# Performance work log

Hardware: AMD Instinct MI355X
Metric: run time of the kernel (lower is better)

The kernel has to match this reference:

```python
import jax, jax.numpy as jnp
import numpy as np

B = 1024
D_FEAT = 64
WINDOW_SIZE = 8192
IR_SIZE = 1024
MAX_STEPS = 2799.0


def setup_inputs() -> dict:
    key = jax.random.key(0)
    ks = jax.random.split(key, 8)
    d_in = D_FEAT + 1  # vel_inputs concat K
    return {
        "vel_inputs": jax.random.normal(ks[0], (B, D_FEAT), dtype=jnp.float32),
        "K": jax.random.uniform(ks[1], (B, 1), dtype=jnp.float32) * MAX_STEPS,
        "eps": jax.random.normal(ks[2], (B, WINDOW_SIZE), dtype=jnp.float32),
        "W_coeff": jax.random.normal(ks[3], (d_in, WINDOW_SIZE), dtype=jnp.float32) * 0.02,
        "b_coeff": jnp.zeros((WINDOW_SIZE,), jnp.float32),
        "W_amps": jax.random.normal(ks[4], (d_in, 1), dtype=jnp.float32) * 0.02,
        "b_amps": jnp.zeros((1,), jnp.float32),
        "W_mean": jax.random.normal(ks[5], (d_in, 1), dtype=jnp.float32) * 0.02,
        "b_mean": jnp.zeros((1,), jnp.float32),
    }


def reference(vel_inputs, K, eps, W_coeff, b_coeff, W_amps, b_amps, W_mean, b_mean):
    # --- small MLP heads ---
    x = jnp.concatenate([vel_inputs, K / MAX_STEPS], axis=-1)  # [B, D+1]
    noise_bands = x @ W_coeff + b_coeff                        # [B, W] (magnitudes)
    amps = jax.nn.sigmoid(x @ W_amps + b_amps)                 # [B, 1]
    mean = jnp.tanh(x @ W_mean + b_mean)                       # [B, 1]

    # --- frequency_impulse_response: irfft + hann windowing (padding>0 branch) ---
    ir = jnp.fft.irfft(noise_bands, axis=-1)   # [B, 2*(W-1)] real
    ir = jnp.fft.fftshift(ir, axes=-1)
    ir_len = 2 * (WINDOW_SIZE - 1)             # 16382
    half = (IR_SIZE + 1) // 2                  # 512
    pad = ir_len - IR_SIZE                     # > 0 path
    n = jnp.arange(IR_SIZE, dtype=jnp.float32)
    hann = 0.5 - 0.5 * jnp.cos(2.0 * jnp.pi * n / IR_SIZE)  # tf periodic hann
    window = jnp.concatenate([hann[half:], jnp.zeros((pad,), jnp.float32), hann[:half]])
    ir = window * ir
    fhs = ir_len - (half - 1) + 1              # first_half_start
    she = half + 1                             # second_half_end
    impulse = jnp.concatenate([ir[:, fhs:], ir[:, :she]], axis=-1)  # [B, IR_SIZE-1]
    ir_final = impulse.shape[-1]               # 1023

    # --- noise generation (eps ~ N(0,1) injected for determinism) ---
    noise = mean + eps                         # [B, W]
    noise = noise / jnp.max(noise)             # global max, as in tf code

    # --- fft_convolve: original broadcasts to [B,B,...] then takes [0];
    # equivalent: noise row 0 convolved with every batch's impulse. ---
    conv_len = ir_final + WINDOW_SIZE - 1
    fft_size = int(2 ** np.ceil(np.log2(conv_len)))  # 16384
    a_fft = jnp.fft.rfft(noise[0], n=fft_size)          # [F]
    ir_fft = jnp.fft.rfft(impulse, n=fft_size, axis=-1)  # [B, F]
    conv = jnp.fft.irfft(a_fft[None, :] * ir_fft, axis=-1)  # [B, fft_size]

    # crop_and_compensate_delay ('same')
    start = (ir_final - 1) // 2 - 1            # 510
    cropped = conv[:, start:start + WINDOW_SIZE]  # [B, W]

    # overlap_and_add over a single frame with step W//2 is the identity
    out_noise = amps * cropped                 # [B, W]
    return out_noise, mean
```

## Files before the change

### kernel.cpp

```cpp
#include <hip/hip_runtime.h>
#include <math.h>

#define NB 1024
#define DF 64
#define WIN 8192
#define LIR 16382
#define TBASE 7681
#define NJ 1024
#define INV_MAXSTEPS (1.0f/2799.0f)
#define TWO_PI 6.28318530717958647692f

#define REVLEN 9248
#define SREV 8212

#define BW_ELEMS 1160
#define BW_CHUNKS 145

using short8 = __attribute__((ext_vector_type(8))) short;
using f32x4  = __attribute__((ext_vector_type(4))) float;

static __device__ __forceinline__ short f2bf(float x) {
    unsigned u = __float_as_uint(x);
    unsigned r = (u + 0x7fffu + ((u >> 16) & 1u)) >> 16;
    return (short)r;
}

__global__ void k_head(const float* __restrict__ vel, const float* __restrict__ Kv,
                       const float* __restrict__ Wa, const float* __restrict__ ba,
                       const float* __restrict__ Wm, const float* __restrict__ bm,
                       float* __restrict__ amps, float* __restrict__ mean,
                       float* __restrict__ out_mean) {
    int b = blockIdx.x * 256 + threadIdx.x;
    if (b >= NB) return;
    float sa = ba[0], sm = bm[0];
    #pragma unroll 8
    for (int d = 0; d < DF; ++d) {
        float v = vel[b * DF + d];
        sa = fmaf(v, Wa[d], sa);
        sm = fmaf(v, Wm[d], sm);
    }
    float xk = Kv[b] * INV_MAXSTEPS;
    sa = fmaf(xk, Wa[DF], sa);
    sm = fmaf(xk, Wm[DF], sm);
    amps[b] = 1.0f / (1.0f + expf(-sa));
    float m = tanhf(sm);
    mean[b] = m;
    out_mean[b] = m;
}

#define PREP_CT_BLK 4096
#define PREP_W_BLK  320
__global__ __launch_bounds__(256) void k_prep(const float* __restrict__ Wc,
                                              const float* __restrict__ bc,
                                              short* __restrict__ Ct,
                                              short* __restrict__ Waug) {
    int bx = blockIdx.x, tid = threadIdx.x;
    if (bx < PREP_CT_BLK) {
        int flat = bx * 2048 + tid * 8;
        int j = flat >> 13, k0 = flat & 8191;
        int t = TBASE + j;
        int p = (k0 * t) % LIR;
        float hw = 0.5f - 0.5f * __builtin_amdgcn_cosf((float)(j + 2) * (1.0f / 1024.0f));
        if (j == NJ - 1) hw = 0.0f;
        short8 v;
        #pragma unroll
        for (int e = 0; e < 8; ++e) {
            int k = k0 + e;
            float w = (k == 0 || k == LIR / 2) ? (1.0f / (float)LIR) : (2.0f / (float)LIR);
            float c = __builtin_amdgcn_cosf((float)p * (1.0f / (float)LIR)) * w * hw;
            v[e] = f2bf(c);
            p += t; if (p >= LIR) p -= LIR;
        }
        *(short8*)(Ct + flat) = v;
    } else {
        int flat = (bx - PREP_CT_BLK) * 2048 + tid * 8;
        int d = flat >> 13, k0 = flat & 8191;
        short8 v;
        #pragma unroll
        for (int e = 0; e < 8; ++e) {
            float x = 0.0f;
            if (d < 65)       x = Wc[(size_t)d * WIN + k0 + e];
            else if (d == 65) x = bc[k0 + e];
            v[e] = f2bf(x);
        }
        *(short8*)(Waug + flat) = v;
    }
}

__global__ void k_maxpart(const float* __restrict__ eps, const float* __restrict__ mean,
                          float* __restrict__ pmax) {
    __shared__ float red[256];
    int tid = threadIdx.x;
    float m = -INFINITY;
    const int total4 = NB * WIN / 4;
    const int stride = 1024 * 256;
    const float4* e4 = (const float4*)eps;
    for (int idx = blockIdx.x * 256 + tid; idx < total4; idx += stride) {
        int b = idx >> 11;
        float4 v = e4[idx];
        float mm = fmaxf(fmaxf(v.x, v.y), fmaxf(v.z, v.w));
        m = fmaxf(m, mean[b] + mm);
    }
    red[tid] = m;
    __syncthreads();
    for (int s = 128; s > 0; s >>= 1) {
        if (tid < s) red[tid] = fmaxf(red[tid], red[tid + s]);
        __syncthreads();
    }
    if (tid == 0) pmax[blockIdx.x] = red[0];
}

__global__ void k_gmax(const float* __restrict__ pmax, const float* __restrict__ mean,
                       float* __restrict__ gmb) {
    __shared__ float red[256];
    int tid = threadIdx.x;
    float m = fmaxf(fmaxf(pmax[tid], pmax[tid + 256]),
                    fmaxf(pmax[tid + 512], pmax[tid + 768]));
    red[tid] = m;
    __syncthreads();
    for (int s = 128; s > 0; s >>= 1) {
        if (tid < s) red[tid] = fmaxf(red[tid], red[tid + s]);
        __syncthreads();
    }
    if (tid == 0) { gmb[0] = 1.0f / red[0]; gmb[1] = mean[0]; }
}

__global__ void k_nrevm(const float* __restrict__ gmb, const float* __restrict__ eps,
                        short* __restrict__ revc) {
    int c = blockIdx.y;
    int x = blockIdx.x * 256 + threadIdx.x;
    if (x >= REVLEN) return;
    float inv = gmb[0], m0 = gmb[1];
    int q = 9239 - x - c;
    int mm = q - 517;
    float v = ((unsigned)mm < (unsigned)WIN) ? (m0 + eps[mm]) * inv : 0.0f;
    revc[c * REVLEN + x] = f2bf(v);
}

#define GA_KCH 256
__global__ __launch_bounds__(256) void k_gemmA(const short* __restrict__ Ct,
                                               const short* __restrict__ Waug,
                                               float* __restrict__ Apart) {
    int tid = threadIdx.x;
    int l = tid & 63, w = tid >> 6;
    int lm = l & 15, lg = l >> 4;
    int m0 = blockIdx.x * 128 + w * 32;
    int ky = blockIdx.y;
    int k0 = ky * GA_KCH;

    const short* pa[2];
    #pragma unroll
    for (int mf = 0; mf < 2; ++mf)
        pa[mf] = Ct + (size_t)(m0 + mf * 16 + lm) * WIN + k0 + 8 * lg;
    const short* pb[5];
    #pragma unroll
    for (int nf = 0; nf < 5; ++nf)
        pb[nf] = Waug + (size_t)(nf * 16 + lm) * WIN + k0 + 8 * lg;

    f32x4 acc[2][5];
    #pragma unroll
    for (int mf = 0; mf < 2; ++mf)
        #pragma unroll
        for (int nf = 0; nf < 5; ++nf)
            #pragma unroll
            for (int r = 0; r < 4; ++r) acc[mf][nf][r] = 0.0f;

    #pragma unroll 2
    for (int kk = 0; kk < GA_KCH; kk += 32) {
        short8 a0 = *(const short8*)(pa[0] + kk);
        short8 a1 = *(const short8*)(pa[1] + kk);
        short8 bb[5];
        #pragma unroll
        for (int nf = 0; nf < 5; ++nf) bb[nf] = *(const short8*)(pb[nf] + kk);
        #pragma unroll
        for (int nf = 0; nf < 5; ++nf) {
            acc[0][nf] = __builtin_amdgcn_mfma_f32_16x16x32_bf16(a0, bb[nf], acc[0][nf], 0, 0, 0);
            acc[1][nf] = __builtin_amdgcn_mfma_f32_16x16x32_bf16(a1, bb[nf], acc[1][nf], 0, 0, 0);
        }
    }
    float* base = Apart + (size_t)ky * (NJ * 80);
    #pragma unroll
    for (int mf = 0; mf < 2; ++mf)
        #pragma unroll
        for (int r = 0; r < 4; ++r) {
            int j = m0 + mf * 16 + 4 * lg + r;
            #pragma unroll
            for (int nf = 0; nf < 5; ++nf)
                base[(size_t)j * 80 + nf * 16 + lm] = acc[mf][nf][r];
        }
}

__global__ __launch_bounds__(256) void k_red(const float* __restrict__ Apart,
                                             float* __restrict__ Aimp) {
    int flat = blockIdx.x * 256 + threadIdx.x;
    float s = 0.0f;
    #pragma unroll 8
    for (int ky = 0; ky < 32; ++ky)
        s += Apart[(size_t)ky * (NJ * 80) + flat];
    int j = flat / 80, d = flat - j * 80;
    Aimp[d * NJ + j] = s;
}

__global__ void k_imp(const float* __restrict__ Aimp, const float* __restrict__ vel,
                      const float* __restrict__ Kv, short* __restrict__ imp_bf) {
    int tid = threadIdx.x;
    int b0 = blockIdx.x * 4;
    float acc[4][4];
    #pragma unroll
    for (int bb = 0; bb < 4; ++bb)
        #pragma unroll
        for (int q = 0; q < 4; ++q) acc[bb][q] = 0.0f;
    for (int d = 0; d < 65; ++d) {
        float xv[4];
        #pragma unroll
        for (int bb = 0; bb < 4; ++bb)
            xv[bb] = (d < DF) ? vel[(b0 + bb) * DF + d] : Kv[b0 + bb] * INV_MAXSTEPS;
        #pragma unroll
        for (int q = 0; q < 4; ++q) {
            float av = Aimp[d * NJ + q * 256 + tid];
            #pragma unroll
            for (int bb = 0; bb < 4; ++bb)
                acc[bb][q] = fmaf(xv[bb], av, acc[bb][q]);
        }
    }
    #pragma unroll
    for (int q = 0; q < 4; ++q) {
        float av = Aimp[65 * NJ + q * 256 + tid];
        #pragma unroll
        for (int bb = 0; bb < 4; ++bb)
            imp_bf[(size_t)(b0 + bb) * NJ + q * 256 + tid] = f2bf(acc[bb][q] + av);
    }
}

__global__ __launch_bounds__(256) void k_gemm(const short* __restrict__ imp_bf,
                                              const short* __restrict__ revc,
                                              const float* __restrict__ amps,
                                              float* __restrict__ out) {
    __shared__ short sA[2][128 * 64];
    __shared__ short sB[8 * BW_ELEMS];
    int tid = threadIdx.x;
    int bid = blockIdx.x;
    int m_idx = bid & 7;
    int n_idx = bid >> 3;
    int brow0 = m_idx * 128;
    int icol0 = n_idx * 128;
    int wbase = 8080 - icol0;

    for (int q = tid; q < 8 * BW_CHUNKS; q += 256) {
        int c = q / BW_CHUNKS;
        int u8 = (q - c * BW_CHUNKS) * 8;
        *(float4*)(sB + q * 8) = *(const float4*)(revc + c * REVLEN + wbase + u8);
    }

    float4 st[4];
    #pragma unroll
    for (int it = 0; it < 4; ++it) {
        int q = it * 256 + tid;
        int row = q >> 3, c16 = q & 7;
        st[it] = *(const float4*)(imp_bf + (size_t)(brow0 + row) * NJ + c16 * 8);
    }
    #pragma unroll
    for (int it = 0; it < 4; ++it) {
        int q = it * 256 + tid;
        int row = q >> 3, c16 = q & 7;
        int db = row * 128 + ((c16 * 16) ^ ((row & 7) << 4));
        *(float4*)((char*)sA[0] + db) = st[it];
    }

    int l = tid & 63, w = tid >> 6;
    int wm = w >> 1, wn = w & 1;
    int lm = l & 15, lg = l >> 4;

    int aoff[4][2];
    #pragma unroll
    for (int mf = 0; mf < 4; ++mf)
        #pragma unroll
        for (int kki = 0; kki < 2; ++kki) {
            int row = wm * 64 + mf * 16 + lm;
            int kb = (kki * 32 + 8 * lg) * 2;
            aoff[mf][kki] = row * 64 + ((kb ^ ((row & 7) << 4)) >> 1);
        }
    int boff[4];
    #pragma unroll
    for (int nf = 0; nf < 4; ++nf) {
        int i = icol0 + wn * 64 + nf * 16 + lm;
        int snf = SREV - i;
        int c = snf & 7;
        boff[nf] = c * BW_ELEMS + (snf - c - wbase) + 8 * lg;
    }

    f32x4 acc[4][4];
    #pragma unroll
    for (int mf = 0; mf < 4; ++mf)
        #pragma unroll
        for (int nf = 0; nf < 4; ++nf)
            #pragma unroll
            for (int r = 0; r < 4; ++r) acc[mf][nf][r] = 0.0f;

    int p = 0;
    for (int ch = 0; ch < 16; ++ch) {
        __syncthreads();
        if (ch < 15) {
            int k0n = (ch + 1) * 64;
            #pragma unroll
            for (int it = 0; it < 4; ++it) {
                int q = it * 256 + tid;
                int row = q >> 3, c16 = q & 7;
                st[it] = *(const float4*)(imp_bf + (size_t)(brow0 + row) * NJ + k0n + c16 * 8);
            }
        }
        int k0 = ch * 64;
        #pragma unroll
        for (int kki = 0; kki < 2; ++kki) {
            short8 af[4], bfr[4];
            #pragma unroll
            for (int mf = 0; mf < 4; ++mf)
                af[mf] = *(const short8*)(sA[p] + aoff[mf][kki]);
            #pragma unroll
            for (int nf = 0; nf < 4; ++nf)
                bfr[nf] = *(const short8*)(sB + boff[nf] + k0 + kki * 32);
            #pragma unroll
            for (int mf = 0; mf < 4; ++mf)
                #pragma unroll
                for (int nf = 0; nf < 4; ++nf)
                    acc[mf][nf] = __builtin_amdgcn_mfma_f32_16x16x32_bf16(
                        af[mf], bfr[nf], acc[mf][nf], 0, 0, 0);
        }
        if (ch < 15) {
            #pragma unroll
            for (int it = 0; it < 4; ++it) {
                int q = it * 256 + tid;
                int row = q >> 3, c16 = q & 7;
                int db = row * 128 + ((c16 * 16) ^ ((row & 7) << 4));
                *(float4*)((char*)sA[p ^ 1] + db) = st[it];
            }
        }
        p ^= 1;
    }

    #pragma unroll
    for (int mf = 0; mf < 4; ++mf) {
        #pragma unroll
        for (int r = 0; r < 4; ++r) {
            int row = brow0 + wm * 64 + mf * 16 + 4 * lg + r;
            float a = amps[row];
            #pragma unroll
            for (int nf = 0; nf < 4; ++nf)
                out[(size_t)row * WIN + icol0 + wn * 64 + nf * 16 + lm] = a * acc[mf][nf][r];
        }
    }
}

extern "C" void kernel_launch(void* const* d_in, const int* in_sizes, int n_in,
                              void* d_out, int out_size, void* d_ws, size_t ws_size,
                              hipStream_t stream) {
    const float* vel = (const float*)d_in[0];
    const float* Kv  = (const float*)d_in[1];
    const float* eps = (const float*)d_in[2];
    const float* Wc  = (const float*)d_in[3];
    const float* bc  = (const float*)d_in[4];
    const float* Wa  = (const float*)d_in[5];
    const float* ba  = (const float*)d_in[6];
    const float* Wm  = (const float*)d_in[7];
    const float* bm  = (const float*)d_in[8];
    float* out = (float*)d_out;

    char* ws = (char*)d_ws;
    float* amps   = (float*)(ws + 0);
    float* mean   = (float*)(ws + 4096);
    float* pmax   = (float*)(ws + 8192);
    float* gmb    = (float*)(ws + 12288);
    float* Aimp   = (float*)(ws + 16384);
    short* imp_bf = (short*)(ws + 344064);
    short* Waug   = (short*)(ws + 2441216);
    short* revc   = (short*)(ws + 3751936);

    short* Ct    = (short*)d_out;
    float* Apart = (float*)((char*)d_out + 16777216);

    k_head   <<<dim3(4),                      dim3(256), 0, stream>>>(vel, Kv, Wa, ba, Wm, bm,
                                                                      amps, mean, out + (size_t)NB * WIN);
    k_prep   <<<dim3(PREP_CT_BLK + PREP_W_BLK), dim3(256), 0, stream>>>(Wc, bc, Ct, Waug);
    k_maxpart<<<dim3(1024),                   dim3(256), 0, stream>>>(eps, mean, pmax);
    k_gmax   <<<dim3(1),                      dim3(256), 0, stream>>>(pmax, mean, gmb);
    k_nrevm  <<<dim3(37, 8),                  dim3(256), 0, stream>>>(gmb, eps, revc);
    k_gemmA  <<<dim3(8, 32),                  dim3(256), 0, stream>>>(Ct, Waug, Apart);
    k_red    <<<dim3(320),                    dim3(256), 0, stream>>>(Apart, Aimp);
    k_imp    <<<dim3(256),                    dim3(256), 0, stream>>>(Aimp, vel, Kv, imp_bf);
    k_gemm   <<<dim3(512),                    dim3(256), 0, stream>>>(imp_bf, revc, amps, out);
}
```

Baseline: 165.1 us.

## Fuse head into prep, atomic global max, LDS-staged gemmA with more K-split

```diff
diff --git a/kernel.cpp b/kernel.cpp
--- a/kernel.cpp
+++ b/kernel.cpp
@@ -25,35 +25,23 @@
     return (short)r;
 }
 
-__global__ void k_head(const float* __restrict__ vel, const float* __restrict__ Kv,
-                       const float* __restrict__ Wa, const float* __restrict__ ba,
-                       const float* __restrict__ Wm, const float* __restrict__ bm,
-                       float* __restrict__ amps, float* __restrict__ mean,
-                       float* __restrict__ out_mean) {
-    int b = blockIdx.x * 256 + threadIdx.x;
-    if (b >= NB) return;
-    float sa = ba[0], sm = bm[0];
-    #pragma unroll 8
-    for (int d = 0; d < DF; ++d) {
-        float v = vel[b * DF + d];
-        sa = fmaf(v, Wa[d], sa);
-        sm = fmaf(v, Wm[d], sm);
-    }
-    float xk = Kv[b] * INV_MAXSTEPS;
-    sa = fmaf(xk, Wa[DF], sa);
-    sm = fmaf(xk, Wm[DF], sm);
-    amps[b] = 1.0f / (1.0f + expf(-sa));
-    float m = tanhf(sm);
-    mean[b] = m;
-    out_mean[b] = m;
-}
-
 #define PREP_CT_BLK 4096
 #define PREP_W_BLK  320
+#define PREP_H_BLK  4
 __global__ __launch_bounds__(256) void k_prep(const float* __restrict__ Wc,
                                               const float* __restrict__ bc,
+                                              const float* __restrict__ vel,
+                                              const float* __restrict__ Kv,
+                                              const float* __restrict__ Wa,
+                                              const float* __restrict__ ba,
+                                              const float* __restrict__ Wm,
+                                              const float* __restrict__ bm,
                                               short* __restrict__ Ct,
-                                              short* __restrict__ Waug) {
+                                              short* __restrict__ Waug,
+                                              float* __restrict__ amps,
+                                              float* __restrict__ mean,
+                                              float* __restrict__ out_mean,
+                                              unsigned* __restrict__ gmb) {
     int bx = blockIdx.x, tid = threadIdx.x;
     if (bx < PREP_CT_BLK) {
         int flat = bx * 2048 + tid * 8;
@@ -72,7 +60,7 @@
             p += t; if (p >= LIR) p -= LIR;
         }
         *(short8*)(Ct + flat) = v;
-    } else {
+    } else if (bx < PREP_CT_BLK + PREP_W_BLK) {
         int flat = (bx - PREP_CT_BLK) * 2048 + tid * 8;
         int d = flat >> 13, k0 = flat & 8191;
         short8 v;
@@ -84,11 +72,29 @@
             v[e] = f2bf(x);
         }
         *(short8*)(Waug + flat) = v;
+    } else if (bx < PREP_CT_BLK + PREP_W_BLK + PREP_H_BLK) {
+        int b = (bx - PREP_CT_BLK - PREP_W_BLK) * 256 + tid;
+        float sa = ba[0], sm = bm[0];
+        #pragma unroll 8
+        for (int d = 0; d < DF; ++d) {
+            float v = vel[b * DF + d];
+            sa = fmaf(v, Wa[d], sa);
+            sm = fmaf(v, Wm[d], sm);
+        }
+        float xk = Kv[b] * INV_MAXSTEPS;
+        sa = fmaf(xk, Wa[DF], sa);
+        sm = fmaf(xk, Wm[DF], sm);
+        amps[b] = 1.0f / (1.0f + expf(-sa));
+        float m = tanhf(sm);
+        mean[b] = m;
+        out_mean[b] = m;
+    } else {
+        if (tid == 0) gmb[0] = 0u;
     }
 }
 
 __global__ void k_maxpart(const float* __restrict__ eps, const float* __restrict__ mean,
-                          float* __restrict__ pmax) {
+                          unsigned* __restrict__ gmb) {
     __shared__ float red[256];
     int tid = threadIdx.x;
     float m = -INFINITY;
@@ -107,83 +113,93 @@
         if (tid < s) red[tid] = fmaxf(red[tid], red[tid + s]);
         __syncthreads();
     }
-    if (tid == 0) pmax[blockIdx.x] = red[0];
-}
-
-__global__ void k_gmax(const float* __restrict__ pmax, const float* __restrict__ mean,
-                       float* __restrict__ gmb) {
-    __shared__ float red[256];
-    int tid = threadIdx.x;
-    float m = fmaxf(fmaxf(pmax[tid], pmax[tid + 256]),
-                    fmaxf(pmax[tid + 512], pmax[tid + 768]));
-    red[tid] = m;
-    __syncthreads();
-    for (int s = 128; s > 0; s >>= 1) {
-        if (tid < s) red[tid] = fmaxf(red[tid], red[tid + s]);
-        __syncthreads();
-    }
-    if (tid == 0) { gmb[0] = 1.0f / red[0]; gmb[1] = mean[0]; }
-}
-
-__global__ void k_nrevm(const float* __restrict__ gmb, const float* __restrict__ eps,
-                        short* __restrict__ revc) {
+    if (tid == 0) {
+        unsigned u = __float_as_uint(red[0]);
+        unsigned key = (u & 0x80000000u) ? ~u : (u | 0x80000000u);
+        atomicMax(gmb, key);
+    }
+}
+
+__global__ void k_nrevm(const unsigned* __restrict__ gmb, const float* __restrict__ mean,
+                        const float* __restrict__ eps, short* __restrict__ revc) {
     int c = blockIdx.y;
     int x = blockIdx.x * 256 + threadIdx.x;
     if (x >= REVLEN) return;
-    float inv = gmb[0], m0 = gmb[1];
+    unsigned key = gmb[0];
+    unsigned u = (key & 0x80000000u) ? (key & 0x7FFFFFFFu) : ~key;
+    float inv = 1.0f / __uint_as_float(u);
+    float m0 = mean[0];
     int q = 9239 - x - c;
     int mm = q - 517;
     float v = ((unsigned)mm < (unsigned)WIN) ? (m0 + eps[mm]) * inv : 0.0f;
     revc[c * REVLEN + x] = f2bf(v);
 }
 
-#define GA_KCH 256
 __global__ __launch_bounds__(256) void k_gemmA(const short* __restrict__ Ct,
                                                const short* __restrict__ Waug,
                                                float* __restrict__ Apart) {
+    __shared__ short sA[128 * 128];
+    __shared__ short sB[80 * 128];
     int tid = threadIdx.x;
+    int j0 = blockIdx.x * 128;
+    int ky = blockIdx.y;
+    int k0 = ky * 128;
+
+    #pragma unroll
+    for (int it = 0; it < 8; ++it) {
+        int q = it * 256 + tid;
+        int row = q >> 4, co = q & 15;
+        float4 v = *(const float4*)(Ct + (size_t)(j0 + row) * WIN + k0 + co * 8);
+        int db = row * 256 + ((co * 16) ^ ((row & 7) << 4));
+        *(float4*)((char*)sA + db) = v;
+    }
+    #pragma unroll
+    for (int it = 0; it < 5; ++it) {
+        int q = it * 256 + tid;
+        int row = q >> 4, co = q & 15;
+        float4 v = *(const float4*)(Waug + (size_t)row * WIN + k0 + co * 8);
+        int db = row * 256 + ((co * 16) ^ ((row & 7) << 4));
+        *(float4*)((char*)sB + db) = v;
+    }
+    __syncthreads();
+
     int l = tid & 63, w = tid >> 6;
     int lm = l & 15, lg = l >> 4;
-    int m0 = blockIdx.x * 128 + w * 32;
-    int ky = blockIdx.y;
-    int k0 = ky * GA_KCH;
-
-    const short* pa[2];
+
+    f32x4 acc[2][5];
     #pragma unroll
     for (int mf = 0; mf < 2; ++mf)
-        pa[mf] = Ct + (size_t)(m0 + mf * 16 + lm) * WIN + k0 + 8 * lg;
-    const short* pb[5];
-    #pragma unroll
-    for (int nf = 0; nf < 5; ++nf)
-        pb[nf] = Waug + (size_t)(nf * 16 + lm) * WIN + k0 + 8 * lg;
-
-    f32x4 acc[2][5];
+        #pragma unroll
+        for (int nf = 0; nf < 5; ++nf)
+            #pragma unroll
+            for (int r = 0; r < 4; ++r) acc[mf][nf][r] = 0.0f;
+
+    #pragma unroll
+    for (int kk = 0; kk < 4; ++kk) {
+        int kb = kk * 64 + 16 * lg;
+        short8 a[2], b[5];
+        #pragma unroll
+        for (int mf = 0; mf < 2; ++mf) {
+            int row = w * 32 + mf * 16 + lm;
+            a[mf] = *(const short8*)((char*)sA + row * 256 + (kb ^ ((row & 7) << 4)));
+        }
+        #pragma unroll
+        for (int nf = 0; nf < 5; ++nf) {
+            int d = nf * 16 + lm;
+            b[nf] = *(const short8*)((char*)sB + d * 256 + (kb ^ ((d & 7) << 4)));
+        }
+        #pragma unroll
+        for (int nf = 0; nf < 5; ++nf) {
+            acc[0][nf] = __builtin_amdgcn_mfma_f32_16x16x32_bf16(a[0], b[nf], acc[0][nf], 0, 0, 0);
+            acc[1][nf] = __builtin_amdgcn_mfma_f32_16x16x32_bf16(a[1], b[nf], acc[1][nf], 0, 0, 0);
+        }
+    }
+    float* base = Apart + (size_t)ky * (NJ * 80);
     #pragma unroll
     for (int mf = 0; mf < 2; ++mf)
         #pragma unroll
-        for (int nf = 0; nf < 5; ++nf)
-            #pragma unroll
-            for (int r = 0; r < 4; ++r) acc[mf][nf][r] = 0.0f;
-
-    #pragma unroll 2
-    for (int kk = 0; kk < GA_KCH; kk += 32) {
-        short8 a0 = *(const short8*)(pa[0] + kk);
-        short8 a1 = *(const short8*)(pa[1] + kk);
-        short8 bb[5];
-        #pragma unroll
-        for (int nf = 0; nf < 5; ++nf) bb[nf] = *(const short8*)(pb[nf] + kk);
-        #pragma unroll
-        for (int nf = 0; nf < 5; ++nf) {
-            acc[0][nf] = __builtin_amdgcn_mfma_f32_16x16x32_bf16(a0, bb[nf], acc[0][nf], 0, 0, 0);
-            acc[1][nf] = __builtin_amdgcn_mfma_f32_16x16x32_bf16(a1, bb[nf], acc[1][nf], 0, 0, 0);
-        }
-    }
-    float* base = Apart + (size_t)ky * (NJ * 80);
-    #pragma unroll
-    for (int mf = 0; mf < 2; ++mf)
-        #pragma unroll
         for (int r = 0; r < 4; ++r) {
-            int j = m0 + mf * 16 + 4 * lg + r;
+            int j = j0 + w * 32 + mf * 16 + 4 * lg + r;
             #pragma unroll
             for (int nf = 0; nf < 5; ++nf)
                 base[(size_t)j * 80 + nf * 16 + lm] = acc[mf][nf][r];
@@ -195,7 +211,7 @@
     int flat = blockIdx.x * 256 + threadIdx.x;
     float s = 0.0f;
     #pragma unroll 8
-    for (int ky = 0; ky < 32; ++ky)
+    for (int ky = 0; ky < 64; ++ky)
         s += Apart[(size_t)ky * (NJ * 80) + flat];
     int j = flat / 80, d = flat - j * 80;
     Aimp[d * NJ + j] = s;
@@ -366,26 +382,23 @@
     float* out = (float*)d_out;
 
     char* ws = (char*)d_ws;
-    float* amps   = (float*)(ws + 0);
-    float* mean   = (float*)(ws + 4096);
-    float* pmax   = (float*)(ws + 8192);
-    float* gmb    = (float*)(ws + 12288);
-    float* Aimp   = (float*)(ws + 16384);
-    short* imp_bf = (short*)(ws + 344064);
-    short* Waug   = (short*)(ws + 2441216);
-    short* revc   = (short*)(ws + 3751936);
-
-    short* Ct    = (short*)d_out;
-    float* Apart = (float*)((char*)d_out + 16777216);
-
-    k_head   <<<dim3(4),                      dim3(256), 0, stream>>>(vel, Kv, Wa, ba, Wm, bm,
-                                                                      amps, mean, out + (size_t)NB * WIN);
-    k_prep   <<<dim3(PREP_CT_BLK + PREP_W_BLK), dim3(256), 0, stream>>>(Wc, bc, Ct, Waug);
-    k_maxpart<<<dim3(1024),                   dim3(256), 0, stream>>>(eps, mean, pmax);
-    k_gmax   <<<dim3(1),                      dim3(256), 0, stream>>>(pmax, mean, gmb);
-    k_nrevm  <<<dim3(37, 8),                  dim3(256), 0, stream>>>(gmb, eps, revc);
-    k_gemmA  <<<dim3(8, 32),                  dim3(256), 0, stream>>>(Ct, Waug, Apart);
-    k_red    <<<dim3(320),                    dim3(256), 0, stream>>>(Apart, Aimp);
-    k_imp    <<<dim3(256),                    dim3(256), 0, stream>>>(Aimp, vel, Kv, imp_bf);
-    k_gemm   <<<dim3(512),                    dim3(256), 0, stream>>>(imp_bf, revc, amps, out);
-}
+    float*    amps   = (float*)(ws + 0);
+    float*    mean   = (float*)(ws + 4096);
+    unsigned* gmb    = (unsigned*)(ws + 8192);
+    float*    Aimp   = (float*)(ws + 16384);
+    short*    imp_bf = (short*)(ws + 344064);
+    short*    Waug   = (short*)(ws + 2441216);
+    short*    revc   = (short*)(ws + 3751936);
+    short*    Ct     = (short*)(ws + 4194304);
+    float*    Apart  = (float*)(ws + 20971520);
+
+    k_prep   <<<dim3(PREP_CT_BLK + PREP_W_BLK + PREP_H_BLK + 1), dim3(256), 0, stream>>>(
+                 Wc, bc, vel, Kv, Wa, ba, Wm, bm, Ct, Waug,
+                 amps, mean, out + (size_t)NB * WIN, gmb);
+    k_maxpart<<<dim3(1024),   dim3(256), 0, stream>>>(eps, mean, gmb);
+    k_nrevm  <<<dim3(37, 8),  dim3(256), 0, stream>>>(gmb, mean, eps, revc);
+    k_gemmA  <<<dim3(8, 64),  dim3(256), 0, stream>>>(Ct, Waug, Apart);
+    k_red    <<<dim3(320),    dim3(256), 0, stream>>>(Apart, Aimp);
+    k_imp    <<<dim3(256),    dim3(256), 0, stream>>>(Aimp, vel, Kv, imp_bf);
+    k_gemm   <<<dim3(512),    dim3(256), 0, stream>>>(imp_bf, revc, amps, out);
+}
```

Result: no change. 166.8 us (+1.0%).
